# Kernel optimization log

Hardware: AMD Instinct MI355X
Metric: run time of the kernel (lower is better)

Reference implementation:

```python
import jax, jax.numpy as jnp
import numpy as np

D_MODEL = 512
NUM_HEADS = 8
D_K = D_MODEL // NUM_HEADS


def setup_inputs() -> dict:
    key = jax.random.key(0)
    ks = jax.random.split(key, 9)
    B, N = 4, 2048
    x = jax.random.normal(ks[0], (B, N, D_MODEL), dtype=jnp.float32)
    s = 1.0 / np.sqrt(D_MODEL)
    Wq = jax.random.normal(ks[1], (D_MODEL, D_MODEL), dtype=jnp.float32) * s
    bq = jax.random.normal(ks[2], (D_MODEL,), dtype=jnp.float32) * 0.02
    Wk = jax.random.normal(ks[3], (D_MODEL, D_MODEL), dtype=jnp.float32) * s
    bk = jax.random.normal(ks[4], (D_MODEL,), dtype=jnp.float32) * 0.02
    Wv = jax.random.normal(ks[5], (D_MODEL, D_MODEL), dtype=jnp.float32) * s
    bv = jax.random.normal(ks[6], (D_MODEL,), dtype=jnp.float32) * 0.02
    Wo = jax.random.normal(ks[7], (D_MODEL, D_MODEL), dtype=jnp.float32) * s
    bo = jax.random.normal(ks[8], (D_MODEL,), dtype=jnp.float32) * 0.02
    return {"x": x, "Wq": Wq, "bq": bq, "Wk": Wk, "bk": bk,
            "Wv": Wv, "bv": bv, "Wo": Wo, "bo": bo}


def reference(x, Wq, bq, Wk, bk, Wv, bv, Wo, bo):
    B, N, _ = x.shape
    # project and split heads: [B, H, N, d_k]
    def split_heads(t):
        return t.reshape(B, N, NUM_HEADS, D_K).transpose(0, 2, 1, 3)
    Q = split_heads(x @ Wq + bq)
    K = split_heads(x @ Wk + bk)
    V = split_heads(x @ Wv + bv)
    scale = 1.0 / np.sqrt(D_K)
    scores = jnp.einsum('bhqd,bhkd->bhqk', Q, K) * scale  # [B,H,N,N]
    probs = jax.nn.softmax(scores, axis=-1)
    attn = jnp.einsum('bhqk,bhkd->bhqd', probs, V)
    attn = attn.transpose(0, 2, 1, 3).reshape(B, N, D_MODEL)
    return attn @ Wo + bo
```

## Files before the change

### kernel.cpp

```cpp
#include <hip/hip_runtime.h>
#include <math.h>

#define D_MODEL 512
#define N_SEQ   2048
#define H       8
#define DK      64

typedef __attribute__((ext_vector_type(8)))  short bf16x8;
typedef __attribute__((ext_vector_type(4)))  float f32x4;
typedef __attribute__((ext_vector_type(16))) float f32x16;

__device__ __forceinline__ unsigned short f2b(float f) {
    unsigned int u = __float_as_uint(f);
    u += 0x7FFF + ((u >> 16) & 1);
    return (unsigned short)(u >> 16);
}

__device__ __forceinline__ unsigned int pack2(float lo, float hi) {
#if __has_builtin(__builtin_amdgcn_cvt_pk_bf16_f32)
    typedef __attribute__((ext_vector_type(2))) short bf16x2;
    bf16x2 p = __builtin_amdgcn_cvt_pk_bf16_f32(lo, hi);
    return (unsigned int)(unsigned short)p[0] |
           ((unsigned int)(unsigned short)p[1] << 16);
#else
    return (unsigned int)f2b(lo) | ((unsigned int)f2b(hi) << 16);
#endif
}

__device__ __forceinline__ float fexp2(float x) {
#if __has_builtin(__builtin_amdgcn_exp2f)
    return __builtin_amdgcn_exp2f(x);
#else
    return __expf(x * 0.6931471805599453f);
#endif
}

__global__ void transpose_all(
    const float* __restrict__ W0, const float* __restrict__ W1,
    const float* __restrict__ W2, const float* __restrict__ W3,
    unsigned short* __restrict__ T0, unsigned short* __restrict__ T1,
    unsigned short* __restrict__ T2, unsigned short* __restrict__ T3)
{
    const float* W; unsigned short* Wt;
    if      (blockIdx.z == 0) { W = W0; Wt = T0; }
    else if (blockIdx.z == 1) { W = W1; Wt = T1; }
    else if (blockIdx.z == 2) { W = W2; Wt = T2; }
    else                      { W = W3; Wt = T3; }

    __shared__ float t[32][33];
    const int tx = threadIdx.x, ty = threadIdx.y;
    const int x = blockIdx.x * 32 + tx;
    const int y0 = blockIdx.y * 32;
    for (int i = ty; i < 32; i += 8)
        t[i][tx] = W[(size_t)(y0 + i) * D_MODEL + x];
    __syncthreads();
    const int ox = blockIdx.y * 32 + tx;
    const int oy0 = blockIdx.x * 32;
    for (int i = ty; i < 32; i += 8)
        Wt[(size_t)(oy0 + i) * D_MODEL + ox] = f2b(t[tx][i]);
}

template<int AMODE>
__device__ __forceinline__ void gemm_body(
    const void* __restrict__ Aptr,
    const unsigned short* __restrict__ Wt,
    const float* __restrict__ bias,
    void* __restrict__ out, int mode, int bx, int by)
{
    __shared__ unsigned short As[128][72];
    __shared__ unsigned short Bs[128][72];

    const int tid  = threadIdx.x;
    const int lane = tid & 63, wave = tid >> 6;
    const int m0 = by * 128, n0 = bx * 128;
    const int wm = (wave & 1) * 64, wn = (wave >> 1) * 64;
    const int cn = lane & 15, g = lane >> 4;

    const int srow = tid >> 1;
    const int scol = (tid & 1) * 32;
    const float* Agf = (const float*)Aptr + (size_t)(m0 + srow) * D_MODEL + scol;
    const unsigned short* Agb =
        (const unsigned short*)Aptr + (size_t)(m0 + srow) * D_MODEL + scol;
    const unsigned short* Bg = Wt + (size_t)(n0 + srow) * D_MODEL + scol;

    f32x4 acc[4][4];
    #pragma unroll
    for (int i = 0; i < 4; ++i)
        #pragma unroll
        for (int j = 0; j < 4; ++j)
            acc[i][j] = (f32x4){0.f, 0.f, 0.f, 0.f};

    for (int k0 = 0; k0 < D_MODEL; k0 += 64) {
        bf16x8 av[4], bv[4];
        #pragma unroll
        for (int q = 0; q < 4; ++q) {
            if (AMODE) {
                float4 f0 = *(const float4*)(Agf + k0 + q * 8);
                float4 f1 = *(const float4*)(Agf + k0 + q * 8 + 4);
                unsigned int* pv = (unsigned int*)&av[q];
                pv[0] = pack2(f0.x, f0.y); pv[1] = pack2(f0.z, f0.w);
                pv[2] = pack2(f1.x, f1.y); pv[3] = pack2(f1.z, f1.w);
            } else {
                av[q] = *(const bf16x8*)(Agb + k0 + q * 8);
            }
            bv[q] = *(const bf16x8*)(Bg + k0 + q * 8);
        }
        __syncthreads();
        #pragma unroll
        for (int q = 0; q < 4; ++q) {
            *(bf16x8*)&As[srow][scol + q * 8] = av[q];
            *(bf16x8*)&Bs[srow][scol + q * 8] = bv[q];
        }
        __syncthreads();

        #pragma unroll
        for (int ks = 0; ks < 2; ++ks) {
            bf16x8 af[4], bf[4];
            #pragma unroll
            for (int i = 0; i < 4; ++i)
                af[i] = *(const bf16x8*)&As[wm + i * 16 + cn][ks * 32 + g * 8];
            #pragma unroll
            for (int j = 0; j < 4; ++j)
                bf[j] = *(const bf16x8*)&Bs[wn + j * 16 + cn][ks * 32 + g * 8];
            #pragma unroll
            for (int i = 0; i < 4; ++i)
                #pragma unroll
                for (int j = 0; j < 4; ++j)
                    acc[i][j] = __builtin_amdgcn_mfma_f32_16x16x32_bf16(
                        af[i], bf[j], acc[i][j], 0, 0, 0);
        }
    }

    if (mode == 2) {
        float* o = (float*)out;
        #pragma unroll
        for (int j = 0; j < 4; ++j) {
            const int n = n0 + wn + j * 16 + cn;
            const float bb = bias[n];
            #pragma unroll
            for (int i = 0; i < 4; ++i)
                #pragma unroll
                for (int r = 0; r < 4; ++r) {
                    const int m = m0 + wm + i * 16 + g * 4 + r;
                    o[(size_t)m * D_MODEL + n] = acc[i][j][r] + bb;
                }
        }
    } else if (mode == 0) {
        unsigned short* o = (unsigned short*)out;
        #pragma unroll
        for (int j = 0; j < 4; ++j) {
            const int n = n0 + wn + j * 16 + cn;
            const int h = n >> 6, d = n & 63;
            const float bb = bias[n];
            #pragma unroll
            for (int i = 0; i < 4; ++i)
                #pragma unroll
                for (int r = 0; r < 4; ++r) {
                    const int m = m0 + wm + i * 16 + g * 4 + r;
                    const int b = m >> 11, t = m & (N_SEQ - 1);
                    o[(((size_t)b * H + h) * N_SEQ + t) * DK + d] =
                        f2b(acc[i][j][r] + bb);
                }
        }
    } else {
        unsigned short* o = (unsigned short*)out;
        #pragma unroll
        for (int j = 0; j < 4; ++j) {
            const int n = n0 + wn + j * 16 + cn;
            const int h = n >> 6, d = n & 63;
            const float bb = bias[n];
            #pragma unroll
            for (int i = 0; i < 4; ++i) {
                const int m = m0 + wm + i * 16 + g * 4;
                const int b = m >> 11, t = m & (N_SEQ - 1);
                ushort4 pk;
                pk.x = f2b(acc[i][j][0] + bb);
                pk.y = f2b(acc[i][j][1] + bb);
                pk.z = f2b(acc[i][j][2] + bb);
                pk.w = f2b(acc[i][j][3] + bb);
                *(ushort4*)(o + (((size_t)b * H + h) * DK + d) * N_SEQ + t) = pk;
            }
        }
    }
}

__global__ __launch_bounds__(256) void gemm_qkv(
    const float* __restrict__ x,
    const unsigned short* __restrict__ Wtq,
    const unsigned short* __restrict__ Wtk,
    const unsigned short* __restrict__ Wtv,
    const float* __restrict__ bq, const float* __restrict__ bk,
    const float* __restrict__ bv,
    unsigned short* __restrict__ Qb, unsigned short* __restrict__ Kb,
    unsigned short* __restrict__ Vtb)
{
    const unsigned short* Wt; const float* bias; void* out; int mode;
    if (blockIdx.z == 0)      { Wt = Wtq; bias = bq; out = Qb;  mode = 0; }
    else if (blockIdx.z == 1) { Wt = Wtk; bias = bk; out = Kb;  mode = 0; }
    else                      { Wt = Wtv; bias = bv; out = Vtb; mode = 1; }
    gemm_body<1>(x, Wt, bias, out, mode, blockIdx.x, blockIdx.y);
}

__global__ __launch_bounds__(256) void gemm_o(
    const unsigned short* __restrict__ A,
    const unsigned short* __restrict__ Wt,
    const float* __restrict__ bias, float* __restrict__ out)
{
    gemm_body<0>(A, Wt, bias, out, 2, blockIdx.x, blockIdx.y);
}

__global__ __launch_bounds__(256) void attn_mfma(
    const unsigned short* __restrict__ Q,
    const unsigned short* __restrict__ K,
    const unsigned short* __restrict__ Vt,
    unsigned short* __restrict__ ctx)
{
    __shared__ unsigned short Ks[64][72];
    __shared__ unsigned short Vs[64][72];
    __shared__ unsigned short Ps[4][32][72];

    const int tid = threadIdx.x, lane = tid & 63, wave = tid >> 6;
    const int q0 = blockIdx.x * 128, h = blockIdx.y, b = blockIdx.z;
    const int lq = lane & 31;
    const int hf = lane >> 5;

    const size_t hb = (size_t)b * H + h;
    const unsigned short* Qp = Q  + hb * N_SEQ * DK;
    const unsigned short* Kp = K  + hb * N_SEQ * DK;
    const unsigned short* Vp = Vt + hb * DK * N_SEQ;

    const int qs = q0 + wave * 32;

    bf16x8 qf[4];
    #pragma unroll
    for (int kd = 0; kd < 4; ++kd)
        qf[kd] = *(const bf16x8*)(Qp + (size_t)(qs + lq) * DK + kd * 16 + hf * 8);

    f32x16 O[2], Ol;
    #pragma unroll
    for (int r = 0; r < 16; ++r) { O[0][r] = 0.f; O[1][r] = 0.f; Ol[r] = 0.f; }

    bf16x8 onesA;
    {
        const short v = (lq == 0) ? (short)0x3F80 : (short)0;
        #pragma unroll
        for (int j = 0; j < 8; ++j) onesA[j] = v;
    }

    const int krow = tid >> 2, kcol = (tid & 3) * 16;
    const float SC2 = 0.18033688011112042f;

    for (int j0 = 0; j0 < N_SEQ; j0 += 64) {
        bf16x8 kv0 = *(const bf16x8*)(Kp + (size_t)(j0 + krow) * DK + kcol);
        bf16x8 kv1 = *(const bf16x8*)(Kp + (size_t)(j0 + krow) * DK + kcol + 8);
        bf16x8 vv0 = *(const bf16x8*)(Vp + (size_t)krow * N_SEQ + j0 + kcol);
        bf16x8 vv1 = *(const bf16x8*)(Vp + (size_t)krow * N_SEQ + j0 + kcol + 8);
        __syncthreads();
        *(bf16x8*)&Ks[krow][kcol]     = kv0;
        *(bf16x8*)&Ks[krow][kcol + 8] = kv1;
        *(bf16x8*)&Vs[krow][kcol]     = vv0;
        *(bf16x8*)&Vs[krow][kcol + 8] = vv1;
        __syncthreads();

        f32x16 s0, s1;
        #pragma unroll
        for (int r = 0; r < 16; ++r) { s0[r] = 0.f; s1[r] = 0.f; }
        #pragma unroll
        for (int kd = 0; kd < 4; ++kd) {
            bf16x8 a0 = *(const bf16x8*)&Ks[lq][kd * 16 + hf * 8];
            bf16x8 a1 = *(const bf16x8*)&Ks[32 + lq][kd * 16 + hf * 8];
            s0 = __builtin_amdgcn_mfma_f32_32x32x16_bf16(a0, qf[kd], s0, 0, 0, 0);
            s1 = __builtin_amdgcn_mfma_f32_32x32x16_bf16(a1, qf[kd], s1, 0, 0, 0);
        }

        unsigned int* prow = (unsigned int*)&Ps[wave][lq][0];
        #pragma unroll
        for (int j = 0; j < 8; ++j) {
            const float p0 = fexp2(s0[2 * j]     * SC2);
            const float p1 = fexp2(s0[2 * j + 1] * SC2);
            prow[(j & 1) + 4 * (j >> 1) + 2 * hf] = pack2(p0, p1);
        }
        #pragma unroll
        for (int j = 0; j < 8; ++j) {
            const float p0 = fexp2(s1[2 * j]     * SC2);
            const float p1 = fexp2(s1[2 * j + 1] * SC2);
            prow[16 + (j & 1) + 4 * (j >> 1) + 2 * hf] = pack2(p0, p1);
        }

        #pragma unroll
        for (int ks = 0; ks < 4; ++ks) {
            bf16x8 bp = *(const bf16x8*)&Ps[wave][lq][ks * 16 + hf * 8];
            bf16x8 a0 = *(const bf16x8*)&Vs[lq][ks * 16 + hf * 8];
            bf16x8 a1 = *(const bf16x8*)&Vs[32 + lq][ks * 16 + hf * 8];
            O[0] = __builtin_amdgcn_mfma_f32_32x32x16_bf16(a0, bp, O[0], 0, 0, 0);
            O[1] = __builtin_amdgcn_mfma_f32_32x32x16_bf16(a1, bp, O[1], 0, 0, 0);
            Ol   = __builtin_amdgcn_mfma_f32_32x32x16_bf16(onesA, bp, Ol, 0, 0, 0);
        }
    }

    const float linv = 1.0f / __shfl(Ol[0], lq);

    unsigned int* prow = (unsigned int*)&Ps[wave][lq][0];
    #pragma unroll
    for (int dt = 0; dt < 2; ++dt)
        #pragma unroll
        for (int rp = 0; rp < 8; ++rp) {
            const float v0 = O[dt][2 * rp]     * linv;
            const float v1 = O[dt][2 * rp + 1] * linv;
            prow[16 * dt + (rp & 1) + 4 * (rp >> 1) + 2 * hf] = pack2(v0, v1);
        }

    const int rr = lane >> 1, hh = lane & 1;
    unsigned short* ob = ctx + ((size_t)b * N_SEQ + (q0 + wave * 32 + rr)) * D_MODEL
                             + h * DK + hh * 32;
    #pragma unroll
    for (int t = 0; t < 4; ++t) {
        bf16x8 v = *(const bf16x8*)&Ps[wave][rr][hh * 32 + t * 8];
        *(bf16x8*)(ob + t * 8) = v;
    }
}

extern "C" void kernel_launch(void* const* d_in, const int* in_sizes, int n_in,
                              void* d_out, int out_size, void* d_ws, size_t ws_size,
                              hipStream_t stream)
{
    const float* x  = (const float*)d_in[0];
    const float* Wq = (const float*)d_in[1];
    const float* bq = (const float*)d_in[2];
    const float* Wk = (const float*)d_in[3];
    const float* bk = (const float*)d_in[4];
    const float* Wv = (const float*)d_in[5];
    const float* bv = (const float*)d_in[6];
    const float* Wo = (const float*)d_in[7];
    const float* bo = (const float*)d_in[8];
    float* out = (float*)d_out;

    const int M = in_sizes[0] / D_MODEL;
    const int B = M / N_SEQ;
    const size_t NX = (size_t)M * D_MODEL;
    const size_t NW = (size_t)D_MODEL * D_MODEL;

    unsigned short* Wtq = (unsigned short*)d_ws;
    unsigned short* Wtk = Wtq + NW;
    unsigned short* Wtv = Wtk + NW;
    unsigned short* Wto = Wtv + NW;
    unsigned short* Qb  = Wto + NW;
    unsigned short* Kb  = Qb + NX;
    unsigned short* Vtb = Kb + NX;
    unsigned short* ctx = Vtb + NX;

    transpose_all<<<dim3(16, 16, 4), dim3(32, 8), 0, stream>>>(
        Wq, Wk, Wv, Wo, Wtq, Wtk, Wtv, Wto);

    gemm_qkv<<<dim3(D_MODEL / 128, M / 128, 3), 256, 0, stream>>>(
        x, Wtq, Wtk, Wtv, bq, bk, bv, Qb, Kb, Vtb);
    attn_mfma<<<dim3(N_SEQ / 128, H, B), 256, 0, stream>>>(Qb, Kb, Vtb, ctx);
    gemm_o<<<dim3(D_MODEL / 128, M / 128), 256, 0, stream>>>(ctx, Wto, bo, out);
}
```

Before: 198.9 us.

## Split attention keys across two blocks, keep P in registers, fold scale into Q

Attention now splits the key range in half across twice as many blocks and writes fp32 partial outputs and row sums, which a new reduce kernel combines and normalizes into the bf16 context. P no longer goes through shared memory: the exp values stay in registers and are rearranged with cross-lane shuffles before the PV MFMA. The ones-row MFMA used for the softmax denominator is replaced by a scalar sum. The softmax scale is folded into the Q projection epilogue, whose Q/K writes are made vectorized by swapping the MFMA operands. This raises occupancy and parallelism for the attention stage, at the cost of an extra launch and fp32 partial-result traffic through global memory.

```diff
diff --git a/kernel.cpp b/kernel.cpp
--- a/kernel.cpp
+++ b/kernel.cpp
@@ -5,6 +5,7 @@
 #define N_SEQ   2048
 #define H       8
 #define DK      64
+#define NQT     (N_SEQ / 128)
 
 typedef __attribute__((ext_vector_type(8)))  short bf16x8;
 typedef __attribute__((ext_vector_type(4)))  float f32x4;
@@ -34,6 +35,8 @@
     return __expf(x * 0.6931471805599453f);
 #endif
 }
+
+#define SC2 0.18033688011112042f
 
 __global__ void transpose_all(
     const float* __restrict__ W0, const float* __restrict__ W1,
@@ -60,12 +63,12 @@
         Wt[(size_t)(oy0 + i) * D_MODEL + ox] = f2b(t[tx][i]);
 }
 
-template<int AMODE>
+template<int AMODE, int SWAP>
 __device__ __forceinline__ void gemm_body(
     const void* __restrict__ Aptr,
     const unsigned short* __restrict__ Wt,
     const float* __restrict__ bias,
-    void* __restrict__ out, int mode, int bx, int by)
+    void* __restrict__ out, int mode, int bx, int by, float sc)
 {
     __shared__ unsigned short As[128][72];
     __shared__ unsigned short Bs[128][72];
@@ -125,13 +128,37 @@
             #pragma unroll
             for (int i = 0; i < 4; ++i)
                 #pragma unroll
-                for (int j = 0; j < 4; ++j)
-                    acc[i][j] = __builtin_amdgcn_mfma_f32_16x16x32_bf16(
-                        af[i], bf[j], acc[i][j], 0, 0, 0);
+                for (int j = 0; j < 4; ++j) {
+                    if (SWAP)
+                        acc[i][j] = __builtin_amdgcn_mfma_f32_16x16x32_bf16(
+                            bf[j], af[i], acc[i][j], 0, 0, 0);
+                    else
+                        acc[i][j] = __builtin_amdgcn_mfma_f32_16x16x32_bf16(
+                            af[i], bf[j], acc[i][j], 0, 0, 0);
+                }
         }
     }
 
-    if (mode == 2) {
+    if constexpr (SWAP) {
+        unsigned short* o = (unsigned short*)out;
+        #pragma unroll
+        for (int j = 0; j < 4; ++j) {
+            const int dbase = n0 + wn + j * 16 + g * 4;
+            const int hh = dbase >> 6, dd = dbase & 63;
+            float4 bb = *(const float4*)&bias[dbase];
+            #pragma unroll
+            for (int i = 0; i < 4; ++i) {
+                const int tt = m0 + wm + i * 16 + cn;
+                const int bi = tt >> 11, tok = tt & (N_SEQ - 1);
+                ushort4 pk;
+                pk.x = f2b((acc[i][j][0] + bb.x) * sc);
+                pk.y = f2b((acc[i][j][1] + bb.y) * sc);
+                pk.z = f2b((acc[i][j][2] + bb.z) * sc);
+                pk.w = f2b((acc[i][j][3] + bb.w) * sc);
+                *(ushort4*)(o + (((size_t)bi * H + hh) * N_SEQ + tok) * DK + dd) = pk;
+            }
+        }
+    } else if (mode == 2) {
         float* o = (float*)out;
         #pragma unroll
         for (int j = 0; j < 4; ++j) {
@@ -143,23 +170,6 @@
                 for (int r = 0; r < 4; ++r) {
                     const int m = m0 + wm + i * 16 + g * 4 + r;
                     o[(size_t)m * D_MODEL + n] = acc[i][j][r] + bb;
-                }
-        }
-    } else if (mode == 0) {
-        unsigned short* o = (unsigned short*)out;
-        #pragma unroll
-        for (int j = 0; j < 4; ++j) {
-            const int n = n0 + wn + j * 16 + cn;
-            const int h = n >> 6, d = n & 63;
-            const float bb = bias[n];
-            #pragma unroll
-            for (int i = 0; i < 4; ++i)
-                #pragma unroll
-                for (int r = 0; r < 4; ++r) {
-                    const int m = m0 + wm + i * 16 + g * 4 + r;
-                    const int b = m >> 11, t = m & (N_SEQ - 1);
-                    o[(((size_t)b * H + h) * N_SEQ + t) * DK + d] =
-                        f2b(acc[i][j][r] + bb);
                 }
         }
     } else {
@@ -194,11 +204,12 @@
     unsigned short* __restrict__ Qb, unsigned short* __restrict__ Kb,
     unsigned short* __restrict__ Vtb)
 {
-    const unsigned short* Wt; const float* bias; void* out; int mode;
-    if (blockIdx.z == 0)      { Wt = Wtq; bias = bq; out = Qb;  mode = 0; }
-    else if (blockIdx.z == 1) { Wt = Wtk; bias = bk; out = Kb;  mode = 0; }
-    else                      { Wt = Wtv; bias = bv; out = Vtb; mode = 1; }
-    gemm_body<1>(x, Wt, bias, out, mode, blockIdx.x, blockIdx.y);
+    if (blockIdx.z == 0)
+        gemm_body<1, 1>(x, Wtq, bq, Qb, 0, blockIdx.x, blockIdx.y, SC2);
+    else if (blockIdx.z == 1)
+        gemm_body<1, 1>(x, Wtk, bk, Kb, 0, blockIdx.x, blockIdx.y, 1.0f);
+    else
+        gemm_body<1, 0>(x, Wtv, bv, Vtb, 1, blockIdx.x, blockIdx.y, 1.0f);
 }
 
 __global__ __launch_bounds__(256) void gemm_o(
@@ -206,23 +217,23 @@
     const unsigned short* __restrict__ Wt,
     const float* __restrict__ bias, float* __restrict__ out)
 {
-    gemm_body<0>(A, Wt, bias, out, 2, blockIdx.x, blockIdx.y);
-}
-
-__global__ __launch_bounds__(256) void attn_mfma(
+    gemm_body<0, 0>(A, Wt, bias, out, 2, blockIdx.x, blockIdx.y, 1.0f);
+}
+
+__global__ __launch_bounds__(256, 4) void attn_mfma(
     const unsigned short* __restrict__ Q,
     const unsigned short* __restrict__ K,
     const unsigned short* __restrict__ Vt,
-    unsigned short* __restrict__ ctx)
+    float* __restrict__ Op, float* __restrict__ lp, int nb)
 {
     __shared__ unsigned short Ks[64][72];
     __shared__ unsigned short Vs[64][72];
-    __shared__ unsigned short Ps[4][32][72];
 
     const int tid = threadIdx.x, lane = tid & 63, wave = tid >> 6;
-    const int q0 = blockIdx.x * 128, h = blockIdx.y, b = blockIdx.z;
-    const int lq = lane & 31;
-    const int hf = lane >> 5;
+    const int qt = blockIdx.x, h = blockIdx.y;
+    const int b = blockIdx.z >> 1, sp = blockIdx.z & 1;
+    const int lq = lane & 31, hf = lane >> 5;
+    const int q0 = qt * 128;
 
     const size_t hb = (size_t)b * H + h;
     const unsigned short* Qp = Q  + hb * N_SEQ * DK;
@@ -230,27 +241,20 @@
     const unsigned short* Vp = Vt + hb * DK * N_SEQ;
 
     const int qs = q0 + wave * 32;
-
     bf16x8 qf[4];
     #pragma unroll
     for (int kd = 0; kd < 4; ++kd)
         qf[kd] = *(const bf16x8*)(Qp + (size_t)(qs + lq) * DK + kd * 16 + hf * 8);
 
-    f32x16 O[2], Ol;
+    f32x16 O[2];
     #pragma unroll
-    for (int r = 0; r < 16; ++r) { O[0][r] = 0.f; O[1][r] = 0.f; Ol[r] = 0.f; }
-
-    bf16x8 onesA;
-    {
-        const short v = (lq == 0) ? (short)0x3F80 : (short)0;
-        #pragma unroll
-        for (int j = 0; j < 8; ++j) onesA[j] = v;
-    }
+    for (int r = 0; r < 16; ++r) { O[0][r] = 0.f; O[1][r] = 0.f; }
+    float lacc = 0.f;
 
     const int krow = tid >> 2, kcol = (tid & 3) * 16;
-    const float SC2 = 0.18033688011112042f;
-
-    for (int j0 = 0; j0 < N_SEQ; j0 += 64) {
+    const int j0beg = sp * (N_SEQ / 2);
+
+    for (int j0 = j0beg; j0 < j0beg + N_SEQ / 2; j0 += 64) {
         bf16x8 kv0 = *(const bf16x8*)(Kp + (size_t)(j0 + krow) * DK + kcol);
         bf16x8 kv1 = *(const bf16x8*)(Kp + (size_t)(j0 + krow) * DK + kcol + 8);
         bf16x8 vv0 = *(const bf16x8*)(Vp + (size_t)krow * N_SEQ + j0 + kcol);
@@ -273,50 +277,96 @@
             s1 = __builtin_amdgcn_mfma_f32_32x32x16_bf16(a1, qf[kd], s1, 0, 0, 0);
         }
 
-        unsigned int* prow = (unsigned int*)&Ps[wave][lq][0];
-        #pragma unroll
-        for (int j = 0; j < 8; ++j) {
-            const float p0 = fexp2(s0[2 * j]     * SC2);
-            const float p1 = fexp2(s0[2 * j + 1] * SC2);
-            prow[(j & 1) + 4 * (j >> 1) + 2 * hf] = pack2(p0, p1);
-        }
-        #pragma unroll
-        for (int j = 0; j < 8; ++j) {
-            const float p0 = fexp2(s1[2 * j]     * SC2);
-            const float p1 = fexp2(s1[2 * j + 1] * SC2);
-            prow[16 + (j & 1) + 4 * (j >> 1) + 2 * hf] = pack2(p0, p1);
-        }
+        unsigned int pk0[4][2], pk1[4][2];
+        #pragma unroll
+        for (int c = 0; c < 4; ++c)
+            #pragma unroll
+            for (int p = 0; p < 2; ++p) {
+                pk0[c][p] = pack2(fexp2(s0[4 * c + 2 * p]),
+                                  fexp2(s0[4 * c + 2 * p + 1]));
+                pk1[c][p] = pack2(fexp2(s1[4 * c + 2 * p]),
+                                  fexp2(s1[4 * c + 2 * p + 1]));
+            }
+
+        #pragma unroll
+        for (int c = 0; c < 4; ++c)
+            #pragma unroll
+            for (int p = 0; p < 2; ++p) {
+                lacc += __uint_as_float(pk0[c][p] << 16) +
+                        __uint_as_float(pk0[c][p] & 0xFFFF0000u) +
+                        __uint_as_float(pk1[c][p] << 16) +
+                        __uint_as_float(pk1[c][p] & 0xFFFF0000u);
+            }
 
         #pragma unroll
         for (int ks = 0; ks < 4; ++ks) {
-            bf16x8 bp = *(const bf16x8*)&Ps[wave][lq][ks * 16 + hf * 8];
-            bf16x8 a0 = *(const bf16x8*)&Vs[lq][ks * 16 + hf * 8];
-            bf16x8 a1 = *(const bf16x8*)&Vs[32 + lq][ks * 16 + hf * 8];
-            O[0] = __builtin_amdgcn_mfma_f32_32x32x16_bf16(a0, bp, O[0], 0, 0, 0);
-            O[1] = __builtin_amdgcn_mfma_f32_32x32x16_bf16(a1, bp, O[1], 0, 0, 0);
-            Ol   = __builtin_amdgcn_mfma_f32_32x32x16_bf16(onesA, bp, Ol, 0, 0, 0);
+            const unsigned int (*src)[2] = (ks < 2) ? pk0 : pk1;
+            const int k2 = ks & 1;
+            const unsigned int a0u = src[2 * k2 + hf][0];
+            const unsigned int a1u = src[2 * k2 + hf][1];
+            const unsigned int b0u = src[2 * k2 + 1 - hf][0];
+            const unsigned int b1u = src[2 * k2 + 1 - hf][1];
+            const unsigned int e0 = (unsigned int)__shfl_xor((int)b0u, 32);
+            const unsigned int e1 = (unsigned int)__shfl_xor((int)b1u, 32);
+            bf16x8 bp;
+            unsigned int* bpu = (unsigned int*)&bp;
+            bpu[0] = hf ? e0 : a0u;
+            bpu[1] = hf ? e1 : a1u;
+            bpu[2] = hf ? a0u : e0;
+            bpu[3] = hf ? a1u : e1;
+            bf16x8 va0 = *(const bf16x8*)&Vs[lq][ks * 16 + hf * 8];
+            bf16x8 va1 = *(const bf16x8*)&Vs[32 + lq][ks * 16 + hf * 8];
+            O[0] = __builtin_amdgcn_mfma_f32_32x32x16_bf16(va0, bp, O[0], 0, 0, 0);
+            O[1] = __builtin_amdgcn_mfma_f32_32x32x16_bf16(va1, bp, O[1], 0, 0, 0);
         }
     }
 
-    const float linv = 1.0f / __shfl(Ol[0], lq);
-
-    unsigned int* prow = (unsigned int*)&Ps[wave][lq][0];
+    const size_t pbase =
+        ((((size_t)sp * nb + b) * H + h) * NQT + qt) * (size_t)(64 * 128);
     #pragma unroll
     for (int dt = 0; dt < 2; ++dt)
         #pragma unroll
-        for (int rp = 0; rp < 8; ++rp) {
-            const float v0 = O[dt][2 * rp]     * linv;
-            const float v1 = O[dt][2 * rp + 1] * linv;
-            prow[16 * dt + (rp & 1) + 4 * (rp >> 1) + 2 * hf] = pack2(v0, v1);
-        }
-
-    const int rr = lane >> 1, hh = lane & 1;
-    unsigned short* ob = ctx + ((size_t)b * N_SEQ + (q0 + wave * 32 + rr)) * D_MODEL
-                             + h * DK + hh * 32;
+        for (int r = 0; r < 16; ++r) {
+            const int row = (r & 3) + 8 * (r >> 2) + 4 * hf;
+            Op[pbase + (size_t)(dt * 32 + row) * 128 + wave * 32 + lq] = O[dt][r];
+        }
+    const float lt = lacc + __shfl_xor(lacc, 32);
+    if (hf == 0)
+        lp[(((size_t)sp * nb + b) * H + h) * N_SEQ + q0 + wave * 32 + lq] = lt;
+}
+
+__global__ __launch_bounds__(256) void reduce_ctx(
+    const float* __restrict__ Op, const float* __restrict__ lp,
+    unsigned short* __restrict__ ctx, int nb)
+{
+    __shared__ float R[64][129];
+    const int tid = threadIdx.x;
+    const int qt = blockIdx.x, h = blockIdx.y, b = blockIdx.z;
+    const size_t tile = (size_t)64 * 128;
+    const size_t i0 = (((size_t)b * H + h) * NQT + qt) * tile;
+    const size_t i1 = ((((size_t)nb + b) * H + h) * NQT + qt) * tile;
+
+    #pragma unroll 4
+    for (int u = 0; u < 32; ++u) {
+        const int idx = u * 256 + tid;
+        R[idx >> 7][idx & 127] = Op[i0 + idx] + Op[i1 + idx];
+    }
+    __syncthreads();
+
+    const int q = tid & 127, dh = tid >> 7;
+    const size_t lb = ((size_t)b * H + h) * N_SEQ + qt * 128 + q;
+    const float inv = 1.0f / (lp[lb] + lp[(size_t)nb * H * N_SEQ + lb]);
+
+    unsigned short* orow = ctx + ((size_t)b * N_SEQ + qt * 128 + q) * D_MODEL
+                               + h * DK + dh * 32;
     #pragma unroll
-    for (int t = 0; t < 4; ++t) {
-        bf16x8 v = *(const bf16x8*)&Ps[wave][rr][hh * 32 + t * 8];
-        *(bf16x8*)(ob + t * 8) = v;
+    for (int t2 = 0; t2 < 4; ++t2) {
+        unsigned int w[4];
+        #pragma unroll
+        for (int p = 0; p < 4; ++p)
+            w[p] = pack2(R[dh * 32 + t2 * 8 + 2 * p][q] * inv,
+                         R[dh * 32 + t2 * 8 + 2 * p + 1][q] * inv);
+        *(bf16x8*)(orow + t2 * 8) = *(bf16x8*)w;
     }
 }
 
@@ -336,7 +386,7 @@
     float* out = (float*)d_out;
 
     const int M = in_sizes[0] / D_MODEL;
-    const int B = M / N_SEQ;
+    const int nb = M / N_SEQ;
     const size_t NX = (size_t)M * D_MODEL;
     const size_t NW = (size_t)D_MODEL * D_MODEL;
 
@@ -347,13 +397,16 @@
     unsigned short* Qb  = Wto + NW;
     unsigned short* Kb  = Qb + NX;
     unsigned short* Vtb = Kb + NX;
-    unsigned short* ctx = Vtb + NX;
+    float* Op = (float*)(Vtb + NX);
+    float* lp = Op + (size_t)2 * nb * H * NQT * 8192;
+    unsigned short* ctx = Qb;
 
     transpose_all<<<dim3(16, 16, 4), dim3(32, 8), 0, stream>>>(
         Wq, Wk, Wv, Wo, Wtq, Wtk, Wtv, Wto);
 
     gemm_qkv<<<dim3(D_MODEL / 128, M / 128, 3), 256, 0, stream>>>(
         x, Wtq, Wtk, Wtv, bq, bk, bv, Qb, Kb, Vtb);
-    attn_mfma<<<dim3(N_SEQ / 128, H, B), 256, 0, stream>>>(Qb, Kb, Vtb, ctx);
+    attn_mfma<<<dim3(NQT, H, nb * 2), 256, 0, stream>>>(Qb, Kb, Vtb, Op, lp, nb);
+    reduce_ctx<<<dim3(NQT, H, nb), 256, 0, stream>>>(Op, lp, ctx, nb);
     gemm_o<<<dim3(D_MODEL / 128, M / 128), 256, 0, stream>>>(ctx, Wto, bo, out);
 }
```

New measurement: 217.4 us. 9.3% more time.
